# Kernel tuning notes

Measured on AMD Instinct MI355X. Metric: run time of the kernel, lower is better.

Reference implementation:

```python
import jax, jax.numpy as jnp
import numpy as np

HID = 2048; NH = 16; DQN = 128; DR = 64; DV = 128; QLR = 1536; KVLR = 512
DQ = DQN + DR  # 192
S = 2048; B = 2
EPS = 1e-6; BASE = 10000.0


def rmsnorm(x, w, eps=EPS):
    xf = x.astype(jnp.float32)
    v = jnp.mean(jnp.square(xf), axis=-1, keepdims=True)
    return (xf * jax.lax.rsqrt(v + eps)).astype(x.dtype) * w


def rope_cos_sin(seq_len, dim):
    inv_freq = 1.0 / (BASE ** (jnp.arange(0, dim, 2, dtype=jnp.float32) / dim))
    freqs = jnp.outer(jnp.arange(seq_len, dtype=jnp.float32), inv_freq)  # [s, d/2]
    emb = jnp.concatenate([freqs, freqs], axis=-1)  # [s, d]
    return jnp.cos(emb), jnp.sin(emb)


def rotate_half(x):
    x1, x2 = jnp.split(x, 2, axis=-1)
    return jnp.concatenate([-x2, x1], axis=-1)


def apply_rope(q, k, cos, sin, position_ids):
    # DeepSeek-V2 variant: interleaved-pair reorder before rotate_half
    cos = cos[position_ids][:, None]  # [b,1,s,d]
    sin = sin[position_ids][:, None]

    def deinterleave(x):
        b, h, s, d = x.shape
        return x.reshape(b, h, s, d // 2, 2).transpose(0, 1, 2, 4, 3).reshape(b, h, s, d)

    q = deinterleave(q)
    k = deinterleave(k)
    return q * cos + rotate_half(q) * sin, k * cos + rotate_half(k) * sin


def setup_inputs() -> dict:
    key = jax.random.key(0)
    ks = jax.random.split(key, 8)
    hidden_states = jax.random.normal(ks[0], (S, B, HID), dtype=jnp.float32)
    causal = jnp.tril(jnp.ones((S, S), dtype=bool))
    attention_mask = jnp.where(causal, 0.0, -1e9).astype(jnp.float32)
    attention_mask = jnp.broadcast_to(attention_mask[None, None], (B, 1, S, S)) + 0.0
    position_ids = jnp.broadcast_to(jnp.arange(S, dtype=jnp.int64 if jax.config.jax_enable_x64 else jnp.int32), (B, S)) + 0
    w = 0.02
    wq_a = jax.random.normal(ks[1], (QLR, HID), dtype=jnp.float32) * w
    q_a_ln_w = jnp.ones((QLR,), dtype=jnp.float32)
    wq_b = jax.random.normal(ks[2], (NH * DQ, QLR), dtype=jnp.float32) * w
    wkv_a = jax.random.normal(ks[3], (KVLR + DR, HID), dtype=jnp.float32) * w
    kv_a_ln_w = jnp.ones((KVLR,), dtype=jnp.float32)
    wkv_b = jax.random.normal(ks[4], (NH * (DQN + DV), KVLR), dtype=jnp.float32) * w
    wo = jax.random.normal(ks[5], (HID, NH * DV), dtype=jnp.float32) * w
    return {"hidden_states": hidden_states, "attention_mask": attention_mask,
            "position_ids": position_ids, "wq_a": wq_a, "q_a_ln_w": q_a_ln_w,
            "wq_b": wq_b, "wkv_a": wkv_a, "kv_a_ln_w": kv_a_ln_w,
            "wkv_b": wkv_b, "wo": wo}


def reference(hidden_states, attention_mask, position_ids, wq_a, q_a_ln_w, wq_b,
              wkv_a, kv_a_ln_w, wkv_b, wo):
    s, b, _ = hidden_states.shape
    # low-rank Q projection: a -> RMSNorm -> b
    q = hidden_states @ wq_a.T                      # [s,b,QLR]
    q = rmsnorm(q, q_a_ln_w) @ wq_b.T               # [s,b,NH*DQ]
    q = q.reshape(s, b, NH, DQ).transpose(1, 2, 0, 3)  # [b,h,s,dq]
    q_nope, q_pe = q[..., :DQN], q[..., DQN:]
    # joint compressed KV + shared rope key
    ckv = hidden_states @ wkv_a.T                   # [s,b,KVLR+DR]
    compressed_kv, k_pe = ckv[..., :KVLR], ckv[..., KVLR:]
    k_pe = k_pe.reshape(s, b, 1, DR).transpose(1, 2, 0, 3)  # [b,1,s,dr]
    kv = rmsnorm(compressed_kv, kv_a_ln_w) @ wkv_b.T         # [s,b,NH*(DQN+DV)]
    kv = kv.reshape(s, b, NH, DQN + DV).transpose(1, 2, 0, 3)
    k_nope, v = kv[..., :DQN], kv[..., DQN:]
    # partial-dim RoPE
    cos, sin = rope_cos_sin(s, DR)
    q_pe, k_pe = apply_rope(q_pe, k_pe, cos, sin, position_ids)
    query = jnp.concatenate([q_nope, q_pe], axis=-1)                 # [b,h,s,dq]
    key = jnp.concatenate([k_nope, jnp.broadcast_to(k_pe, (b, NH, s, DR))], axis=-1)
    scale = DQ ** -0.5
    scores = jnp.einsum('bhqd,bhkd->bhqk', query, key) * scale + attention_mask
    attn = jax.nn.softmax(scores.astype(jnp.float32), axis=-1).astype(query.dtype)
    out = jnp.einsum('bhqk,bhkd->bhqd', attn, v)    # [b,h,s,dv]
    out = out.transpose(2, 0, 1, 3).reshape(s, b, NH * DV)
    return out @ wo.T                               # [s,b,HID]
```

## Files before the change

### kernel.cpp

```cpp
#include <hip/hip_runtime.h>
#include <cmath>

typedef unsigned short u16;
typedef __bf16 bf16x8 __attribute__((ext_vector_type(8)));
typedef float f32x4 __attribute__((ext_vector_type(4)));

#define MFMA16(a,b,c) __builtin_amdgcn_mfma_f32_16x16x32_bf16((a),(b),(c),0,0,0)

__device__ __forceinline__ u16 f2bf(float f){
  union { float f; unsigned u; } x; x.f = f;
  unsigned r = x.u + 0x7FFFu + ((x.u >> 16) & 1u);
  return (u16)(r >> 16);
}
__device__ __forceinline__ float bf2f(u16 v){
  union { unsigned u; float f; } x; x.u = ((unsigned)v) << 16; return x.f;
}
__device__ __forceinline__ void gload16(const void* g, void* l){
  __builtin_amdgcn_global_load_lds((const __attribute__((address_space(1))) void*)g,
                                   (__attribute__((address_space(3))) void*)l, 16, 0, 0);
}
__device__ __forceinline__ float block_sum256(float v, float* red, int tid){
  #pragma unroll
  for (int off = 32; off; off >>= 1) v += __shfl_xor(v, off);
  if ((tid & 63) == 0) red[tid >> 6] = v;
  __syncthreads();
  return red[0] + red[1] + red[2] + red[3];
}

__global__ __launch_bounds__(256) void k_conv(const float* __restrict__ in,
                                              u16* __restrict__ out, int n4){
  int i = blockIdx.x * 256 + threadIdx.x;
  int stride = gridDim.x * 256;
  for (; i < n4; i += stride){
    float4 v = reinterpret_cast<const float4*>(in)[i];
    ushort4 o; o.x = f2bf(v.x); o.y = f2bf(v.y); o.z = f2bf(v.z); o.w = f2bf(v.w);
    reinterpret_cast<ushort4*>(out)[i] = o;
  }
}

__global__ __launch_bounds__(256) void k_convw(const float* __restrict__ s0,
                                               const float* __restrict__ s1,
                                               const float* __restrict__ s2,
                                               const float* __restrict__ s3,
                                               u16* __restrict__ d0, u16* __restrict__ d1,
                                               u16* __restrict__ d2, u16* __restrict__ d3){
  const int n0 = 1536 * 2048 / 4, n1 = 3072 * 1536 / 4;
  const int n2 = 4096 * 512 / 4,  n3 = 2048 * 2048 / 4;
  const int total = n0 + n1 + n2 + n3;
  const float SCL2 = 0.104117549f;
  int i = blockIdx.x * 256 + threadIdx.x;
  int stride = gridDim.x * 256;
  for (; i < total; i += stride){
    const float* s; u16* d; int j = i; float m = 1.f;
    if (j < n0){ s = s0; d = d0; }
    else if ((j -= n0) < n1){ s = s1; d = d1; m = SCL2; }
    else if ((j -= n1) < n2){ s = s2; d = d2; }
    else { j -= n2; s = s3; d = d3; }
    float4 v = reinterpret_cast<const float4*>(s)[j];
    ushort4 o; o.x = f2bf(v.x * m); o.y = f2bf(v.y * m);
    o.z = f2bf(v.z * m); o.w = f2bf(v.w * m);
    reinterpret_cast<ushort4*>(d)[j] = o;
  }
}

__global__ __launch_bounds__(256) void k_conv_kva(const float* __restrict__ in,
                                                  u16* __restrict__ out){
  const int n4 = 640 * 2048 / 4;
  int i = blockIdx.x * 256 + threadIdx.x;
  int stride = gridDim.x * 256;
  for (; i < n4; i += stride){
    int e = i * 4; int row = e >> 11; int col = e & 2047;
    ushort4 o;
    if (row < 576){
      float4 v = *reinterpret_cast<const float4*>(in + (size_t)row * 2048 + col);
      o.x = f2bf(v.x); o.y = f2bf(v.y); o.z = f2bf(v.z); o.w = f2bf(v.w);
    } else { o.x = 0; o.y = 0; o.z = 0; o.w = 0; }
    reinterpret_cast<ushort4*>(out)[i] = o;
  }
}

template<int OUT_BF16>
__global__ __launch_bounds__(256) void k_gemm(const u16* __restrict__ A,
                                              const u16* __restrict__ Bm,
                                              void* __restrict__ Cv,
                                              int M, int N, int K){
  __shared__ __align__(16) u16 sA[2][128 * 32];
  __shared__ __align__(16) u16 sB[2][128 * 32];
  const int tid = threadIdx.x, w = tid >> 6, l = tid & 63;
  const int ln = l & 15, lg = l >> 4;
  const int id  = blockIdx.x + gridDim.x * blockIdx.y;
  const int nwg = gridDim.x * gridDim.y;
  const int swz = (id & 7) * (nwg >> 3) + (id >> 3);
  const int bx  = swz & (gridDim.x - 1);
  const int by  = swz / gridDim.x;
  const int m0 = bx * 128, n0 = by * 128;
  const int wr = w >> 1, wc = w & 1;
  const int trow = tid >> 2, tcol = (tid & 3) * 8;

  const f32x4 zf = {0.f, 0.f, 0.f, 0.f};
  f32x4 acc[4][4];
  #pragma unroll
  for (int i = 0; i < 4; ++i)
    #pragma unroll
    for (int j = 0; j < 4; ++j) acc[i][j] = zf;

  const u16* ga = A  + (size_t)(m0 + trow) * K + tcol;
  const u16* gb = Bm + (size_t)(n0 + trow) * K + tcol;
  const int nk = K >> 5;

  #define GSTAGE(kt_, bi_) {                                   \
    char* la_ = (char*)sA[bi_] + w * 1024;                     \
    char* lb_ = (char*)sB[bi_] + w * 1024;                     \
    gload16(ga + (kt_) * 32,                  la_);            \
    gload16(ga + (kt_) * 32 + (size_t)64 * K, la_ + 4096);     \
    gload16(gb + (kt_) * 32,                  lb_);            \
    gload16(gb + (kt_) * 32 + (size_t)64 * K, lb_ + 4096);     \
  }

  GSTAGE(0, 0);
  __syncthreads();

  for (int kt = 0; kt < nk; ++kt){
    const int bi = kt & 1;
    if (kt + 1 < nk) GSTAGE(kt + 1, bi ^ 1);

    bf16x8 af[4], bfr[4];
    #pragma unroll
    for (int i = 0; i < 4; ++i)
      af[i] = *(const bf16x8*)&sA[bi][(wr * 64 + i * 16 + ln) * 32 + lg * 8];
    #pragma unroll
    for (int j = 0; j < 4; ++j)
      bfr[j] = *(const bf16x8*)&sB[bi][(wc * 64 + j * 16 + ln) * 32 + lg * 8];
    #pragma unroll
    for (int i = 0; i < 4; ++i)
      #pragma unroll
      for (int j = 0; j < 4; ++j)
        acc[i][j] = MFMA16(af[i], bfr[j], acc[i][j]);

    __syncthreads();
  }
  #undef GSTAGE

  const int mb = m0 + wr * 64, nb = n0 + wc * 64;
  #pragma unroll
  for (int i = 0; i < 4; ++i)
    #pragma unroll
    for (int j = 0; j < 4; ++j)
      #pragma unroll
      for (int r = 0; r < 4; ++r){
        int mm = mb + i * 16 + lg * 4 + r;
        int nn = nb + j * 16 + ln;
        if (OUT_BF16) ((u16*)Cv)[(size_t)mm * N + nn] = f2bf(acc[i][j][r]);
        else          ((float*)Cv)[(size_t)mm * N + nn] = acc[i][j][r];
      }
}

__global__ __launch_bounds__(256) void k_rms_fused(const float* __restrict__ in,
                                                   const float* __restrict__ wq,
                                                   const float* __restrict__ wkv,
                                                   u16* __restrict__ outq,
                                                   u16* __restrict__ outkv,
                                                   u16* __restrict__ kpe){
  __shared__ float red[4];
  const int row = blockIdx.x, tid = threadIdx.x;
  const float* x = in + (size_t)row * 2176;
  float ss = 0.f;
  #pragma unroll
  for (int i = tid; i < 1536; i += 256){ float v = x[i]; ss += v * v; }
  float tot = block_sum256(ss, red, tid);
  float inv = rsqrtf(tot * (1.f / 1536.f) + 1e-6f);
  #pragma unroll
  for (int i = tid; i < 1536; i += 256)
    outq[(size_t)row * 1536 + i] = f2bf(x[i] * inv * wq[i]);
  __syncthreads();
  const float* y = x + 1536;
  float v0 = y[tid], v1 = y[tid + 256];
  float tot2 = block_sum256(v0 * v0 + v1 * v1, red, tid);
  float inv2 = rsqrtf(tot2 * (1.f / 512.f) + 1e-6f);
  outkv[(size_t)row * 512 + tid]       = f2bf(v0 * inv2 * wkv[tid]);
  outkv[(size_t)row * 512 + tid + 256] = f2bf(v1 * inv2 * wkv[tid + 256]);
  if (tid < 32){
    int j = tid;
    float e = y[512 + 2 * j], o = y[512 + 2 * j + 1];
    float pos  = (float)(row >> 1);
    float invf = exp2f(-13.287712379549449f * (float)j * (1.f / 32.f));
    float th = pos * invf, sn = sinf(th), cs = cosf(th);
    kpe[(size_t)row * 64 + j]      = f2bf(e * cs - o * sn);
    kpe[(size_t)row * 64 + 32 + j] = f2bf(o * cs + e * sn);
  }
}

__global__ __launch_bounds__(64) void k_rope_q(const u16* __restrict__ q,
                                               u16* __restrict__ qpe){
  const int sb = blockIdx.x;
  const int h  = blockIdx.y * 2 + (threadIdx.x >> 5);
  const int j  = threadIdx.x & 31;
  const u16* base = q + (size_t)sb * 3072 + h * 192 + 128;
  float e = bf2f(base[2 * j]), o = bf2f(base[2 * j + 1]);
  float pos  = (float)(sb >> 1);
  float invf = exp2f(-13.287712379549449f * (float)j * (1.f / 32.f));
  float th = pos * invf, sn = sinf(th), cs = cosf(th);
  u16* dst = qpe + ((size_t)sb * 16 + h) * 64;
  dst[j]      = f2bf(e * cs - o * sn);
  dst[32 + j] = f2bf(o * cs + e * sn);
}

__global__ __launch_bounds__(256) void k_vtrans(const u16* __restrict__ kv,
                                                u16* __restrict__ vt){
  __shared__ u16 t[64][65];
  const int bh = blockIdx.z, b = bh >> 4, h = bh & 15;
  const int s0 = blockIdx.x * 64, d0 = blockIdx.y * 64;
  const int tid = threadIdx.x;
  #pragma unroll
  for (int i = 0; i < 16; ++i){
    int idx = i * 256 + tid; int si = idx >> 6, di = idx & 63;
    t[si][di] = kv[(size_t)((s0 + si) * 2 + b) * 4096 + h * 256 + 128 + d0 + di];
  }
  __syncthreads();
  #pragma unroll
  for (int i = 0; i < 16; ++i){
    int idx = i * 256 + tid; int di = idx >> 6, si = idx & 63;
    vt[(size_t)((b * 16 + h) * 128 + d0 + di) * 2048 + s0 + si] = t[si][di];
  }
}

__global__ __launch_bounds__(256, 2) void k_attn(const u16* __restrict__ q,
                                                 const u16* __restrict__ qpe,
                                                 const u16* __restrict__ kv,
                                                 const u16* __restrict__ kpe,
                                                 const u16* __restrict__ vt,
                                                 u16* __restrict__ out){
  const int i_ = blockIdx.x + 8 * (blockIdx.y + 16 * blockIdx.z);
  const int j_ = i_ >> 3, x_ = i_ & 7;
  const int g_ = x_ * 4 + (j_ >> 3);
  const int bx = j_ & 7;
  const int h = g_ & 15, b = g_ >> 4;
  const int bh = b * 16 + h;
  const int tid = threadIdx.x, w = tid >> 6, l = tid & 63;
  const int ln = l & 15, lg = l >> 4;

  __shared__ __align__(16) u16 sK[2][64 * 128];
  __shared__ __align__(16) u16 sPE[2][64 * 64];
  __shared__ __align__(16) u16 sV[2][128 * 64];

  const f32x4 zf = {0.f, 0.f, 0.f, 0.f};

  #define PERM(pr_) ((((pr_) >> 5) << 5) + ((((pr_) >> 2) & 3) << 3) + \
                     ((((pr_) >> 4) & 1) << 2) + ((pr_) & 3))
  #define STAGE(kt_, bi_) {                                                     \
    _Pragma("unroll")                                                           \
    for (int p = 0; p < 4; ++p){                                                \
      int o_ = p * 4096 + tid * 16;                                             \
      int pr = o_ >> 8, cl = (o_ >> 4) & 15, cg = cl ^ (pr & 7);                \
      int kl = PERM(pr);                                                        \
      gload16(kv + (size_t)(((kt_) * 64 + kl) * 2 + b) * 4096 + h * 256 + cg * 8, \
              (char*)sK[bi_] + o_);                                             \
    }                                                                           \
    _Pragma("unroll")                                                           \
    for (int p = 0; p < 2; ++p){                                                \
      int o_ = p * 4096 + tid * 16;                                             \
      int pr = o_ >> 7, cl = (o_ >> 4) & 7, cg = cl ^ (pr & 7);                 \
      int kl = PERM(pr);                                                        \
      gload16(kpe + (size_t)(((kt_) * 64 + kl) * 2 + b) * 64 + cg * 8,          \
              (char*)sPE[bi_] + o_);                                            \
    }                                                                           \
    _Pragma("unroll")                                                           \
    for (int p = 0; p < 4; ++p){                                                \
      int o_ = p * 4096 + tid * 16;                                             \
      int row = o_ >> 7, cl = (o_ >> 4) & 7, cg = cl ^ (row & 7);               \
      gload16(vt + (size_t)(bh * 128 + row) * 2048 + (kt_) * 64 + cg * 8,       \
              (char*)sV[bi_] + o_);                                             \
    } }

  for (int half = 0; half < 2; ++half){
    const int qt = half ? (15 - bx) : bx;
    const int row0 = qt * 128 + w * 32;

    bf16x8 qf[2][6];
    #pragma unroll
    for (int rb = 0; rb < 2; ++rb){
      int sq = row0 + rb * 16 + ln;
      const u16* qr = q + (size_t)(sq * 2 + b) * 3072 + h * 192;
      #pragma unroll
      for (int kb = 0; kb < 4; ++kb) qf[rb][kb] = *(const bf16x8*)(qr + kb * 32 + lg * 8);
      const u16* pr_ = qpe + ((size_t)(sq * 2 + b) * 16 + h) * 64;
      qf[rb][4] = *(const bf16x8*)(pr_ + lg * 8);
      qf[rb][5] = *(const bf16x8*)(pr_ + 32 + lg * 8);
    }

    f32x4 o[2][8];
    float m_i[2] = {-3.0e38f, -3.0e38f}, l_i[2] = {0.f, 0.f};
    #pragma unroll
    for (int rb = 0; rb < 2; ++rb)
      #pragma unroll
      for (int c8 = 0; c8 < 8; ++c8) o[rb][c8] = zf;

    const int nkt = 2 * qt + 2;
    STAGE(0, 0);
    __syncthreads();

    for (int kt = 0; kt < nkt; ++kt){
      const int bi = kt & 1;
      if (kt + 1 < nkt) STAGE(kt + 1, bi ^ 1);

      if (kt * 64 <= row0 + 31){
        f32x4 s_[2][4];
        #pragma unroll
        for (int cb = 0; cb < 4; ++cb){
          int rl = cb * 16 + ln, swz = rl & 7;
          bf16x8 kf[6];
          #pragma unroll
          for (int kb = 0; kb < 4; ++kb)
            kf[kb] = *(const bf16x8*)((char*)sK[bi] + rl * 256 + (((kb * 4 + lg) ^ swz) << 4));
          kf[4] = *(const bf16x8*)((char*)sPE[bi] + rl * 128 + ((lg ^ swz) << 4));
          kf[5] = *(const bf16x8*)((char*)sPE[bi] + rl * 128 + (((4 + lg) ^ swz) << 4));
          #pragma unroll
          for (int rb = 0; rb < 2; ++rb){
            f32x4 acc = zf;
            #pragma unroll
            for (int kb = 0; kb < 6; ++kb)
              acc = MFMA16(kf[kb], qf[rb][kb], acc);
            s_[rb][cb] = acc;
          }
        }

        bf16x8 pa[2][2];
        #pragma unroll
        for (int rb = 0; rb < 2; ++rb){
          const int sqv = row0 + rb * 16 + ln;
          const bool needMask = (kt * 64 + 63) > (row0 + rb * 16);
          float mx = -3.0e38f;
          #pragma unroll
          for (int cb = 0; cb < 4; ++cb)
            #pragma unroll
            for (int r = 0; r < 4; ++r){
              float v = s_[rb][cb][r];
              if (needMask){
                int sk = kt * 64 + 32 * (cb >> 1) + 8 * lg + 4 * (cb & 1) + r;
                v = (sk <= sqv) ? v : -3.0e38f;
              }
              s_[rb][cb][r] = v;
              mx = fmaxf(mx, v);
            }
          mx = fmaxf(mx, __shfl_xor(mx, 16));
          mx = fmaxf(mx, __shfl_xor(mx, 32));
          if (!__all(mx <= m_i[rb] + 11.6f)){
            float mn = fmaxf(m_i[rb], mx);
            float sf = exp2f(m_i[rb] - mn);
            m_i[rb] = mn;
            l_i[rb] *= sf;
            float sf0 = __shfl(sf, 4 * lg + 0);
            float sf1 = __shfl(sf, 4 * lg + 1);
            float sf2 = __shfl(sf, 4 * lg + 2);
            float sf3 = __shfl(sf, 4 * lg + 3);
            #pragma unroll
            for (int c8 = 0; c8 < 8; ++c8){
              o[rb][c8][0] *= sf0; o[rb][c8][1] *= sf1;
              o[rb][c8][2] *= sf2; o[rb][c8][3] *= sf3;
            }
          }
          float rs = 0.f;
          #pragma unroll
          for (int cb = 0; cb < 4; ++cb)
            #pragma unroll
            for (int r = 0; r < 4; ++r){
              float p = exp2f(s_[rb][cb][r] - m_i[rb]);
              s_[rb][cb][r] = p;
              rs += p;
            }
          rs += __shfl_xor(rs, 16);
          rs += __shfl_xor(rs, 32);
          l_i[rb] += rs;

          #pragma unroll
          for (int hf = 0; hf < 2; ++hf){
            unsigned pw0, pw1, pw2, pw3;
            f32x4 sa = s_[rb][hf * 2], sb2 = s_[rb][hf * 2 + 1];
            asm("v_cvt_pk_bf16_f32 %0, %1, %2" : "=v"(pw0) : "v"(sa[0]),  "v"(sa[1]));
            asm("v_cvt_pk_bf16_f32 %0, %1, %2" : "=v"(pw1) : "v"(sa[2]),  "v"(sa[3]));
            asm("v_cvt_pk_bf16_f32 %0, %1, %2" : "=v"(pw2) : "v"(sb2[0]), "v"(sb2[1]));
            asm("v_cvt_pk_bf16_f32 %0, %1, %2" : "=v"(pw3) : "v"(sb2[2]), "v"(sb2[3]));
            union { uint4 u; bf16x8 v; } pk;
            pk.u.x = pw0; pk.u.y = pw1; pk.u.z = pw2; pk.u.w = pw3;
            pa[rb][hf] = pk.v;
          }
        }

        #pragma unroll
        for (int c8 = 0; c8 < 8; ++c8){
          int d = c8 * 16 + ln, swz = d & 7;
          bf16x8 vf0 = *(const bf16x8*)((char*)sV[bi] + d * 128 + ((lg ^ swz) << 4));
          bf16x8 vf1 = *(const bf16x8*)((char*)sV[bi] + d * 128 + (((4 + lg) ^ swz) << 4));
          #pragma unroll
          for (int rb = 0; rb < 2; ++rb){
            o[rb][c8] = MFMA16(pa[rb][0], vf0, o[rb][c8]);
            o[rb][c8] = MFMA16(pa[rb][1], vf1, o[rb][c8]);
          }
        }
      }
      __syncthreads();
    }

    #pragma unroll
    for (int rb = 0; rb < 2; ++rb){
      float li0 = __shfl(l_i[rb], 4 * lg + 0);
      float li1 = __shfl(l_i[rb], 4 * lg + 1);
      float li2 = __shfl(l_i[rb], 4 * lg + 2);
      float li3 = __shfl(l_i[rb], 4 * lg + 3);
      float iv0 = 1.f / li0, iv1 = 1.f / li1, iv2 = 1.f / li2, iv3 = 1.f / li3;
      int sqr = row0 + rb * 16 + lg * 4;
      #pragma unroll
      for (int c8 = 0; c8 < 8; ++c8){
        int col = h * 128 + c8 * 16 + ln;
        out[(size_t)((sqr + 0) * 2 + b) * 2048 + col] = f2bf(o[rb][c8][0] * iv0);
        out[(size_t)((sqr + 1) * 2 + b) * 2048 + col] = f2bf(o[rb][c8][1] * iv1);
        out[(size_t)((sqr + 2) * 2 + b) * 2048 + col] = f2bf(o[rb][c8][2] * iv2);
        out[(size_t)((sqr + 3) * 2 + b) * 2048 + col] = f2bf(o[rb][c8][3] * iv3);
      }
    }
  }
  #undef STAGE
  #undef PERM
}

extern "C" void kernel_launch(void* const* d_in, const int* in_sizes, int n_in,
                              void* d_out, int out_size, void* d_ws, size_t ws_size,
                              hipStream_t stream){
  const float* hidden    = (const float*)d_in[0];
  const float* wq_a      = (const float*)d_in[3];
  const float* q_a_ln_w  = (const float*)d_in[4];
  const float* wq_b      = (const float*)d_in[5];
  const float* wkv_a     = (const float*)d_in[6];
  const float* kv_a_ln_w = (const float*)d_in[7];
  const float* wkv_b     = (const float*)d_in[8];
  const float* wo        = (const float*)d_in[9];

  char* ws = (char*)d_ws;
  size_t off = 0;
  auto alloc = [&](size_t bytes){ size_t o = off; off += (bytes + 255) & ~(size_t)255; return o; };
  const size_t SB = 4096;

  u16*   hid_bf   = (u16*)(ws + alloc(SB * 2048 * 2));
  u16*   wqab_bf  = (u16*)(ws + alloc((size_t)2176 * 2048 * 2));
  u16*   wqb_bf   = (u16*)(ws + alloc((size_t)3072 * 1536 * 2));
  u16*   wkvb_bf  = (u16*)(ws + alloc((size_t)4096 * 512 * 2));
  u16*   wo_bf    = (u16*)(ws + alloc((size_t)2048 * 2048 * 2));
  float* qa_f     = (float*)(ws + alloc(SB * 2176 * 4));
  u16*   qrms_bf  = (u16*)(ws + alloc(SB * 1536 * 2));
  u16*   ckvr_bf  = (u16*)(ws + alloc(SB * 512 * 2));
  u16*   kpe_bf   = (u16*)(ws + alloc(SB * 64 * 2));
  u16*   qfull_bf = (u16*)(ws + alloc(SB * 3072 * 2));
  u16*   qpe_bf   = (u16*)(ws + alloc(SB * 16 * 64 * 2));
  u16*   kv_bf    = (u16*)(ws + alloc(SB * 4096 * 2));
  u16*   vt_bf    = hid_bf;
  u16*   attn_bf  = (u16*)qa_f;

  dim3 blk(256);
  k_conv<<<2048, blk, 0, stream>>>(hidden, hid_bf, (int)(SB * 2048 / 4));
  k_convw<<<2048, blk, 0, stream>>>(wq_a, wq_b, wkv_b, wo,
                                    wqab_bf, wqb_bf, wkvb_bf, wo_bf);
  k_conv_kva<<<512, blk, 0, stream>>>(wkv_a, wqab_bf + (size_t)1536 * 2048);
  k_gemm<0><<<dim3(32, 17), blk, 0, stream>>>(hid_bf, wqab_bf, qa_f, 4096, 2176, 2048);
  k_rms_fused<<<4096, blk, 0, stream>>>(qa_f, q_a_ln_w, kv_a_ln_w, qrms_bf, ckvr_bf, kpe_bf);
  k_gemm<1><<<dim3(32, 24), blk, 0, stream>>>(qrms_bf, wqb_bf, qfull_bf, 4096, 3072, 1536);
  k_rope_q<<<dim3(4096, 8), dim3(64), 0, stream>>>(qfull_bf, qpe_bf);
  k_gemm<1><<<dim3(32, 32), blk, 0, stream>>>(ckvr_bf, wkvb_bf, kv_bf, 4096, 4096, 512);
  k_vtrans<<<dim3(32, 2, 32), blk, 0, stream>>>(kv_bf, vt_bf);
  k_attn<<<dim3(8, 16, 2), blk, 0, stream>>>(qfull_bf, qpe_bf, kv_bf, kpe_bf, vt_bf, attn_bf);
  k_gemm<0><<<dim3(32, 16), blk, 0, stream>>>(attn_bf, wo_bf, d_out, 4096, 2048, 2048);
}
```

Before: 342.0 us.

## Fuse query RoPE into attention and shrink attention tiles to 64x32

Removes the separate query-RoPE kernel. The rms kernel now writes a cos/sin table, and the attention kernel applies RoPE to the query's positional slice when it loads it into registers. The attention kernel also moves to 128-thread blocks covering 64 query rows, with 32-key tiles and half the shared memory, doubling the grid. This saves a launch and an intermediate buffer round trip, and should give finer causal skipping and more blocks in flight. The cost is more synchronisation per key, smaller MFMA batches per barrier, and extra RoPE math per block.

```diff
diff --git a/kernel.cpp b/kernel.cpp
--- a/kernel.cpp
+++ b/kernel.cpp
@@ -4,6 +4,7 @@
 typedef unsigned short u16;
 typedef __bf16 bf16x8 __attribute__((ext_vector_type(8)));
 typedef float f32x4 __attribute__((ext_vector_type(4)));
+typedef unsigned short us8 __attribute__((ext_vector_type(8)));
 
 #define MFMA16(a,b,c) __builtin_amdgcn_mfma_f32_16x16x32_bf16((a),(b),(c),0,0,0)
 
@@ -160,7 +161,8 @@
                                                    const float* __restrict__ wkv,
                                                    u16* __restrict__ outq,
                                                    u16* __restrict__ outkv,
-                                                   u16* __restrict__ kpe){
+                                                   u16* __restrict__ kpe,
+                                                   float* __restrict__ cs_tab){
   __shared__ float red[4];
   const int row = blockIdx.x, tid = threadIdx.x;
   const float* x = in + (size_t)row * 2176;
@@ -187,22 +189,9 @@
     float th = pos * invf, sn = sinf(th), cs = cosf(th);
     kpe[(size_t)row * 64 + j]      = f2bf(e * cs - o * sn);
     kpe[(size_t)row * 64 + 32 + j] = f2bf(o * cs + e * sn);
-  }
-}
-
-__global__ __launch_bounds__(64) void k_rope_q(const u16* __restrict__ q,
-                                               u16* __restrict__ qpe){
-  const int sb = blockIdx.x;
-  const int h  = blockIdx.y * 2 + (threadIdx.x >> 5);
-  const int j  = threadIdx.x & 31;
-  const u16* base = q + (size_t)sb * 3072 + h * 192 + 128;
-  float e = bf2f(base[2 * j]), o = bf2f(base[2 * j + 1]);
-  float pos  = (float)(sb >> 1);
-  float invf = exp2f(-13.287712379549449f * (float)j * (1.f / 32.f));
-  float th = pos * invf, sn = sinf(th), cs = cosf(th);
-  u16* dst = qpe + ((size_t)sb * 16 + h) * 64;
-  dst[j]      = f2bf(e * cs - o * sn);
-  dst[32 + j] = f2bf(o * cs + e * sn);
+    cs_tab[(size_t)row * 64 + j]      = cs;
+    cs_tab[(size_t)row * 64 + 32 + j] = sn;
+  }
 }
 
 __global__ __launch_bounds__(256) void k_vtrans(const u16* __restrict__ kv,
@@ -224,68 +213,83 @@
   }
 }
 
-__global__ __launch_bounds__(256, 2) void k_attn(const u16* __restrict__ q,
-                                                 const u16* __restrict__ qpe,
+__global__ __launch_bounds__(128, 2) void k_attn(const u16* __restrict__ q,
                                                  const u16* __restrict__ kv,
                                                  const u16* __restrict__ kpe,
                                                  const u16* __restrict__ vt,
+                                                 const float* __restrict__ cs_tab,
                                                  u16* __restrict__ out){
-  const int i_ = blockIdx.x + 8 * (blockIdx.y + 16 * blockIdx.z);
+  const int i_ = blockIdx.x + 16 * (blockIdx.y + 16 * blockIdx.z);
   const int j_ = i_ >> 3, x_ = i_ & 7;
-  const int g_ = x_ * 4 + (j_ >> 3);
-  const int bx = j_ & 7;
+  const int g_ = x_ * 4 + (j_ >> 4);
+  const int bx = j_ & 15;
   const int h = g_ & 15, b = g_ >> 4;
   const int bh = b * 16 + h;
   const int tid = threadIdx.x, w = tid >> 6, l = tid & 63;
   const int ln = l & 15, lg = l >> 4;
 
-  __shared__ __align__(16) u16 sK[2][64 * 128];
-  __shared__ __align__(16) u16 sPE[2][64 * 64];
-  __shared__ __align__(16) u16 sV[2][128 * 64];
+  __shared__ __align__(16) u16 sK[2][32 * 128];
+  __shared__ __align__(16) u16 sPE[2][32 * 64];
+  __shared__ __align__(16) u16 sV[2][128 * 32];
 
   const f32x4 zf = {0.f, 0.f, 0.f, 0.f};
 
-  #define PERM(pr_) ((((pr_) >> 5) << 5) + ((((pr_) >> 2) & 3) << 3) + \
-                     ((((pr_) >> 4) & 1) << 2) + ((pr_) & 3))
+  #define PERM(pr_) (((((pr_) >> 2) & 3) << 3) + ((((pr_) >> 4) & 1) << 2) + ((pr_) & 3))
   #define STAGE(kt_, bi_) {                                                     \
     _Pragma("unroll")                                                           \
     for (int p = 0; p < 4; ++p){                                                \
-      int o_ = p * 4096 + tid * 16;                                             \
+      int o_ = p * 2048 + tid * 16;                                             \
       int pr = o_ >> 8, cl = (o_ >> 4) & 15, cg = cl ^ (pr & 7);                \
       int kl = PERM(pr);                                                        \
-      gload16(kv + (size_t)(((kt_) * 64 + kl) * 2 + b) * 4096 + h * 256 + cg * 8, \
+      gload16(kv + (size_t)(((kt_) * 32 + kl) * 2 + b) * 4096 + h * 256 + cg * 8, \
               (char*)sK[bi_] + o_);                                             \
     }                                                                           \
     _Pragma("unroll")                                                           \
     for (int p = 0; p < 2; ++p){                                                \
-      int o_ = p * 4096 + tid * 16;                                             \
+      int o_ = p * 2048 + tid * 16;                                             \
       int pr = o_ >> 7, cl = (o_ >> 4) & 7, cg = cl ^ (pr & 7);                 \
       int kl = PERM(pr);                                                        \
-      gload16(kpe + (size_t)(((kt_) * 64 + kl) * 2 + b) * 64 + cg * 8,          \
+      gload16(kpe + (size_t)(((kt_) * 32 + kl) * 2 + b) * 64 + cg * 8,          \
               (char*)sPE[bi_] + o_);                                            \
     }                                                                           \
     _Pragma("unroll")                                                           \
     for (int p = 0; p < 4; ++p){                                                \
-      int o_ = p * 4096 + tid * 16;                                             \
-      int row = o_ >> 7, cl = (o_ >> 4) & 7, cg = cl ^ (row & 7);               \
-      gload16(vt + (size_t)(bh * 128 + row) * 2048 + (kt_) * 64 + cg * 8,       \
+      int o_ = p * 2048 + tid * 16;                                             \
+      int row = o_ >> 6, ch = (o_ >> 4) & 3, cg = ch ^ (row & 3);               \
+      gload16(vt + (size_t)(bh * 128 + row) * 2048 + (kt_) * 32 + cg * 8,       \
               (char*)sV[bi_] + o_);                                             \
     } }
 
   for (int half = 0; half < 2; ++half){
-    const int qt = half ? (15 - bx) : bx;
-    const int row0 = qt * 128 + w * 32;
+    const int qt = half ? (31 - bx) : bx;
+    const int qrow0 = qt * 64 + w * 32;
 
     bf16x8 qf[2][6];
     #pragma unroll
     for (int rb = 0; rb < 2; ++rb){
-      int sq = row0 + rb * 16 + ln;
+      int sq = qrow0 + rb * 16 + ln;
       const u16* qr = q + (size_t)(sq * 2 + b) * 3072 + h * 192;
       #pragma unroll
       for (int kb = 0; kb < 4; ++kb) qf[rb][kb] = *(const bf16x8*)(qr + kb * 32 + lg * 8);
-      const u16* pr_ = qpe + ((size_t)(sq * 2 + b) * 16 + h) * 64;
-      qf[rb][4] = *(const bf16x8*)(pr_ + lg * 8);
-      qf[rb][5] = *(const bf16x8*)(pr_ + 32 + lg * 8);
+      u16 rawa[16];
+      *(us8*)&rawa[0] = *(const us8*)(qr + 128 + 16 * lg);
+      *(us8*)&rawa[8] = *(const us8*)(qr + 128 + 16 * lg + 8);
+      const float* ct = cs_tab + (size_t)(sq * 2 + b) * 64 + 8 * lg;
+      float cc[8], ss_[8];
+      *(float4*)&cc[0]  = *(const float4*)(ct);
+      *(float4*)&cc[4]  = *(const float4*)(ct + 4);
+      *(float4*)&ss_[0] = *(const float4*)(ct + 32);
+      *(float4*)&ss_[4] = *(const float4*)(ct + 36);
+      union { u16 s[8]; bf16x8 v; } pe4, pe5;
+      #pragma unroll
+      for (int i2 = 0; i2 < 8; ++i2){
+        float e  = bf2f(rawa[2 * i2]);
+        float o2 = bf2f(rawa[2 * i2 + 1]);
+        pe4.s[i2] = f2bf(e * cc[i2] - o2 * ss_[i2]);
+        pe5.s[i2] = f2bf(o2 * cc[i2] + e * ss_[i2]);
+      }
+      qf[rb][4] = pe4.v;
+      qf[rb][5] = pe5.v;
     }
 
     f32x4 o[2][8];
@@ -303,10 +307,10 @@
       const int bi = kt & 1;
       if (kt + 1 < nkt) STAGE(kt + 1, bi ^ 1);
 
-      if (kt * 64 <= row0 + 31){
-        f32x4 s_[2][4];
+      if (kt * 32 <= qrow0 + 31){
+        f32x4 s_[2][2];
         #pragma unroll
-        for (int cb = 0; cb < 4; ++cb){
+        for (int cb = 0; cb < 2; ++cb){
           int rl = cb * 16 + ln, swz = rl & 7;
           bf16x8 kf[6];
           #pragma unroll
@@ -324,19 +328,19 @@
           }
         }
 
-        bf16x8 pa[2][2];
+        bf16x8 pa[2];
         #pragma unroll
         for (int rb = 0; rb < 2; ++rb){
-          const int sqv = row0 + rb * 16 + ln;
-          const bool needMask = (kt * 64 + 63) > (row0 + rb * 16);
+          const int sqv = qrow0 + rb * 16 + ln;
+          const bool needMask = (kt * 32 + 31) > (qrow0 + rb * 16);
           float mx = -3.0e38f;
           #pragma unroll
-          for (int cb = 0; cb < 4; ++cb)
+          for (int cb = 0; cb < 2; ++cb)
             #pragma unroll
             for (int r = 0; r < 4; ++r){
               float v = s_[rb][cb][r];
               if (needMask){
-                int sk = kt * 64 + 32 * (cb >> 1) + 8 * lg + 4 * (cb & 1) + r;
+                int sk = kt * 32 + 8 * lg + 4 * cb + r;
                 v = (sk <= sqv) ? v : -3.0e38f;
               }
               s_[rb][cb][r] = v;
@@ -361,7 +365,7 @@
           }
           float rs = 0.f;
           #pragma unroll
-          for (int cb = 0; cb < 4; ++cb)
+          for (int cb = 0; cb < 2; ++cb)
             #pragma unroll
             for (int r = 0; r < 4; ++r){
               float p = exp2f(s_[rb][cb][r] - m_i[rb]);
@@ -372,30 +376,24 @@
           rs += __shfl_xor(rs, 32);
           l_i[rb] += rs;
 
-          #pragma unroll
-          for (int hf = 0; hf < 2; ++hf){
-            unsigned pw0, pw1, pw2, pw3;
-            f32x4 sa = s_[rb][hf * 2], sb2 = s_[rb][hf * 2 + 1];
-            asm("v_cvt_pk_bf16_f32 %0, %1, %2" : "=v"(pw0) : "v"(sa[0]),  "v"(sa[1]));
-            asm("v_cvt_pk_bf16_f32 %0, %1, %2" : "=v"(pw1) : "v"(sa[2]),  "v"(sa[3]));
-            asm("v_cvt_pk_bf16_f32 %0, %1, %2" : "=v"(pw2) : "v"(sb2[0]), "v"(sb2[1]));
-            asm("v_cvt_pk_bf16_f32 %0, %1, %2" : "=v"(pw3) : "v"(sb2[2]), "v"(sb2[3]));
-            union { uint4 u; bf16x8 v; } pk;
-            pk.u.x = pw0; pk.u.y = pw1; pk.u.z = pw2; pk.u.w = pw3;
-            pa[rb][hf] = pk.v;
-          }
+          unsigned pw0, pw1, pw2, pw3;
+          f32x4 sa = s_[rb][0], sb2 = s_[rb][1];
+          asm("v_cvt_pk_bf16_f32 %0, %1, %2" : "=v"(pw0) : "v"(sa[0]),  "v"(sa[1]));
+          asm("v_cvt_pk_bf16_f32 %0, %1, %2" : "=v"(pw1) : "v"(sa[2]),  "v"(sa[3]));
+          asm("v_cvt_pk_bf16_f32 %0, %1, %2" : "=v"(pw2) : "v"(sb2[0]), "v"(sb2[1]));
+          asm("v_cvt_pk_bf16_f32 %0, %1, %2" : "=v"(pw3) : "v"(sb2[2]), "v"(sb2[3]));
+          union { uint4 u; bf16x8 v; } pk;
+          pk.u.x = pw0; pk.u.y = pw1; pk.u.z = pw2; pk.u.w = pw3;
+          pa[rb] = pk.v;
         }
 
         #pragma unroll
         for (int c8 = 0; c8 < 8; ++c8){
-          int d = c8 * 16 + ln, swz = d & 7;
-          bf16x8 vf0 = *(const bf16x8*)((char*)sV[bi] + d * 128 + ((lg ^ swz) << 4));
-          bf16x8 vf1 = *(const bf16x8*)((char*)sV[bi] + d * 128 + (((4 + lg) ^ swz) << 4));
+          int d = c8 * 16 + ln;
+          bf16x8 vf = *(const bf16x8*)((char*)sV[bi] + d * 64 + ((lg ^ (d & 3)) << 4));
           #pragma unroll
-          for (int rb = 0; rb < 2; ++rb){
-            o[rb][c8] = MFMA16(pa[rb][0], vf0, o[rb][c8]);
-            o[rb][c8] = MFMA16(pa[rb][1], vf1, o[rb][c8]);
-          }
+          for (int rb = 0; rb < 2; ++rb)
+            o[rb][c8] = MFMA16(pa[rb], vf, o[rb][c8]);
         }
       }
       __syncthreads();
@@ -408,7 +406,7 @@
       float li2 = __shfl(l_i[rb], 4 * lg + 2);
       float li3 = __shfl(l_i[rb], 4 * lg + 3);
       float iv0 = 1.f / li0, iv1 = 1.f / li1, iv2 = 1.f / li2, iv3 = 1.f / li3;
-      int sqr = row0 + rb * 16 + lg * 4;
+      int sqr = qrow0 + rb * 16 + lg * 4;
       #pragma unroll
       for (int c8 = 0; c8 < 8; ++c8){
         int col = h * 128 + c8 * 16 + ln;
@@ -449,8 +447,8 @@
   u16*   qrms_bf  = (u16*)(ws + alloc(SB * 1536 * 2));
   u16*   ckvr_bf  = (u16*)(ws + alloc(SB * 512 * 2));
   u16*   kpe_bf   = (u16*)(ws + alloc(SB * 64 * 2));
+  float* cs_f     = (float*)(ws + alloc(SB * 64 * 4));
   u16*   qfull_bf = (u16*)(ws + alloc(SB * 3072 * 2));
-  u16*   qpe_bf   = (u16*)(ws + alloc(SB * 16 * 64 * 2));
   u16*   kv_bf    = (u16*)(ws + alloc(SB * 4096 * 2));
   u16*   vt_bf    = hid_bf;
   u16*   attn_bf  = (u16*)qa_f;
@@ -461,11 +459,12 @@
                                     wqab_bf, wqb_bf, wkvb_bf, wo_bf);
   k_conv_kva<<<512, blk, 0, stream>>>(wkv_a, wqab_bf + (size_t)1536 * 2048);
   k_gemm<0><<<dim3(32, 17), blk, 0, stream>>>(hid_bf, wqab_bf, qa_f, 4096, 2176, 2048);
-  k_rms_fused<<<4096, blk, 0, stream>>>(qa_f, q_a_ln_w, kv_a_ln_w, qrms_bf, ckvr_bf, kpe_bf);
+  k_rms_fused<<<4096, blk, 0, stream>>>(qa_f, q_a_ln_w, kv_a_ln_w, qrms_bf, ckvr_bf,
+                                        kpe_bf, cs_f);
   k_gemm<1><<<dim3(32, 24), blk, 0, stream>>>(qrms_bf, wqb_bf, qfull_bf, 4096, 3072, 1536);
-  k_rope_q<<<dim3(4096, 8), dim3(64), 0, stream>>>(qfull_bf, qpe_bf);
   k_gemm<1><<<dim3(32, 32), blk, 0, stream>>>(ckvr_bf, wkvb_bf, kv_bf, 4096, 4096, 512);
   k_vtrans<<<dim3(32, 2, 32), blk, 0, stream>>>(kv_bf, vt_bf);
-  k_attn<<<dim3(8, 16, 2), blk, 0, stream>>>(qfull_bf, qpe_bf, kv_bf, kpe_bf, vt_bf, attn_bf);
+  k_attn<<<dim3(16, 16, 2), dim3(128), 0, stream>>>(qfull_bf, kv_bf, kpe_bf, vt_bf,
+                                                    cs_f, attn_bf);
   k_gemm<0><<<dim3(32, 16), blk, 0, stream>>>(attn_bf, wo_bf, d_out, 4096, 2048, 2048);
 }
```

Result: slower. 364.7 us (+6.7%).
